# Kernel optimization log

Measured on AMD Instinct MI355X. Metric: run time of the kernel, lower is better.

Reference implementation:

```python
import jax, jax.numpy as jnp
import numpy as np

NQ = 4  # circuit is hard-wired to a 4-qubit ring
INV_SQRT2 = 1.0 / float(np.sqrt(2.0))


def _apply_1q(state, g, w):
    # state: [E,2,2,2,2]; g: [2,2] (shared) or [E,2,2] (per-edge)
    state = jnp.moveaxis(state, 1 + w, -1)
    sub = 'eab,e...b->e...a' if g.ndim == 3 else 'ab,e...b->e...a'
    state = jnp.einsum(sub, g, state)
    return jnp.moveaxis(state, -1, 1 + w)


def _apply_cry(state, theta, c, t):
    # controlled-RY(theta) with control wire c, target wire t; theta: [E]
    st = jnp.moveaxis(state, (1 + c, 1 + t), (-2, -1))  # [..., c, t]
    co = jnp.cos(theta / 2)[:, None, None]
    si = jnp.sin(theta / 2)[:, None, None]
    a = st[..., 1, 0]
    b = st[..., 1, 1]
    n0 = co * a - si * b
    n1 = si * a + co * b
    st = jnp.stack([jnp.stack([st[..., 0, 0], st[..., 0, 1]], axis=-1),
                    jnp.stack([n0, n1], axis=-1)], axis=-2)
    return jnp.moveaxis(st, (-2, -1), (1 + c, 1 + t))


def _simulate(q, k, params):
    # q, k: [E, NQ] rotation angles; params: [NQ, 3]
    E = q.shape[0]
    state = jnp.zeros((E, 2 ** NQ), jnp.complex64).at[:, 0].set(1.0)
    state = state.reshape((E,) + (2,) * NQ)
    # RY(query[i]) on wire i
    for w in range(NQ):
        c = jnp.cos(q[:, w] / 2)
        s = jnp.sin(q[:, w] / 2)
        g = jnp.stack([jnp.stack([c, -s], -1), jnp.stack([s, c], -1)], -2)
        state = _apply_1q(state, g.astype(jnp.complex64), w)
    # Hadamard on all wires
    H = jnp.array([[1, 1], [1, -1]], jnp.complex64) * INV_SQRT2
    for w in range(NQ):
        state = _apply_1q(state, H, w)
    # CRY(key[i]) on (i, (i+1)%NQ)
    for w in range(NQ):
        state = _apply_cry(state, k[:, w], w, (w + 1) % NQ)
    # Rot(phi, theta, omega) = RZ(omega) RY(theta) RZ(phi) on each wire
    for w in range(NQ):
        phi, th, om = params[w, 0], params[w, 1], params[w, 2]
        ct = jnp.cos(th / 2)
        st_ = jnp.sin(th / 2)
        g = jnp.stack([
            jnp.stack([jnp.exp(-1j * (phi + om) / 2) * ct, -jnp.exp(1j * (phi - om) / 2) * st_]),
            jnp.stack([jnp.exp(-1j * (phi - om) / 2) * st_, jnp.exp(1j * (phi + om) / 2) * ct]),
        ]).astype(jnp.complex64)
        state = _apply_1q(state, g, w)
    # <Z_i> expectation values
    p = jnp.abs(state) ** 2  # [E,2,2,2,2] float32
    exps = []
    for i in range(NQ):
        axes = tuple(a for a in range(1, 1 + NQ) if a != 1 + i)
        m = p.sum(axes)  # [E, 2]
        exps.append(m[:, 0] - m[:, 1])
    return jnp.stack(exps, -1).mean(-1)  # [E]


def setup_inputs() -> dict:
    key = jax.random.key(0)
    ks = jax.random.split(key, 7)
    N, D, E = 50000, 256, 800000
    node_features = jax.random.normal(ks[0], (N, D), jnp.float32)
    edge_index = jax.random.randint(ks[1], (2, E), 0, N)
    Wq = jax.random.normal(ks[2], (NQ, D), jnp.float32) / np.float32(np.sqrt(D))
    bq = jnp.zeros((NQ,), jnp.float32)
    Wk = jax.random.normal(ks[3], (NQ, D), jnp.float32) / np.float32(np.sqrt(D))
    bk = jnp.zeros((NQ,), jnp.float32)
    quantum_params = jax.random.normal(ks[4], (NQ, 3), jnp.float32) * 0.1
    return {'node_features': node_features, 'edge_index': edge_index,
            'Wq': Wq, 'bq': bq, 'Wk': Wk, 'bk': bk,
            'quantum_params': quantum_params}


def reference(node_features, edge_index, Wq, bq, Wk, bk, quantum_params):
    half_pi = np.float32(np.pi / 2)
    queries = jnp.tanh(node_features @ Wq.T + bq) * half_pi  # [N, NQ]
    keys = jnp.tanh(node_features @ Wk.T + bk) * half_pi     # [N, NQ]
    qe = queries[edge_index[0]]  # [E, NQ]
    ke = keys[edge_index[1]]     # [E, NQ]
    attn = _simulate(qe, ke, quantum_params)  # [E]
    return jax.nn.softmax(attn, axis=0)
```

## Files before the change

kernel.cpp:

```cpp
#include <hip/hip_runtime.h>
#include <math.h>

#define HALF_PI   1.57079632679489662f
#define INV_SQRT2 0.70710678118654752f
#define NPART     1024

__global__ __launch_bounds__(256) void node_qk(
        const float* __restrict__ feat,
        const float* __restrict__ Wq, const float* __restrict__ bq,
        const float* __restrict__ Wk, const float* __restrict__ bk,
        float* __restrict__ qtab, float* __restrict__ ktab, int N) {
    const int lane  = threadIdx.x & 63;
    const int wid   = (int)((blockIdx.x * blockDim.x + threadIdx.x) >> 6);
    const int nwid  = (int)((gridDim.x * blockDim.x) >> 6);

    float4 wq4[4], wk4[4];
    #pragma unroll
    for (int q = 0; q < 4; ++q) {
        wq4[q] = reinterpret_cast<const float4*>(Wq + q * 256)[lane];
        wk4[q] = reinterpret_cast<const float4*>(Wk + q * 256)[lane];
    }
    const int  g    = lane >> 3;
    const float bias = (g < 4) ? bq[g] : bk[g & 3];

    const bool hi  = (lane & 32) != 0;
    const bool s16 = (lane & 16) != 0;
    const bool s8  = (lane & 8)  != 0;

    for (int n = wid; n < N; n += nwid) {
        float4 f = reinterpret_cast<const float4*>(feat)[(size_t)n * 64 + lane];
        float acc[8];
        #pragma unroll
        for (int q = 0; q < 4; ++q) {
            acc[q]     = f.x * wq4[q].x + f.y * wq4[q].y + f.z * wq4[q].z + f.w * wq4[q].w;
            acc[4 + q] = f.x * wk4[q].x + f.y * wk4[q].y + f.z * wk4[q].z + f.w * wk4[q].w;
        }

        #pragma unroll
        for (int j = 0; j < 4; ++j) {
            float give = hi ? acc[j] : acc[j + 4];
            float r = __shfl_xor(give, 32, 64);
            acc[j]     += hi ? 0.f : r;
            acc[j + 4] += hi ? r : 0.f;
        }
        #pragma unroll
        for (int j = 0; j < 2; ++j) {
            float giveLow  = hi ? acc[6 + j] : acc[2 + j];
            float giveHigh = hi ? acc[4 + j] : acc[j];
            float give = s16 ? giveHigh : giveLow;
            float r = __shfl_xor(give, 16, 64);
            acc[j]     += (!hi && !s16) ? r : 0.f;
            acc[2 + j] += (!hi &&  s16) ? r : 0.f;
            acc[4 + j] += ( hi && !s16) ? r : 0.f;
            acc[6 + j] += ( hi &&  s16) ? r : 0.f;
        }
        float a_even = hi ? (s16 ? acc[6] : acc[4]) : (s16 ? acc[2] : acc[0]);
        float a_odd  = hi ? (s16 ? acc[7] : acc[5]) : (s16 ? acc[3] : acc[1]);
        float give3 = s8 ? a_even : a_odd;
        float r3 = __shfl_xor(give3, 8, 64);
        float v = (s8 ? a_odd : a_even) + r3;
        v += __shfl_xor(v, 4, 64);
        v += __shfl_xor(v, 2, 64);
        v += __shfl_xor(v, 1, 64);

        if ((lane & 7) == 0) {
            float t = tanhf(v + bias) * HALF_PI;
            if (g < 4) qtab[(size_t)n * 4 + g] = t;
            else       ktab[(size_t)n * 4 + (g & 3)] = t;
        }
    }
}

__global__ __launch_bounds__(256) void edge_attn(
        const int* __restrict__ ei,
        const float4* __restrict__ qtab, const float4* __restrict__ ktab,
        const float* __restrict__ qp,
        float* __restrict__ out, float* __restrict__ partial, int E) {
    __shared__ float scz[4], scx[4];
    __shared__ float red[256];
    const int tid = threadIdx.x;
    if (tid < 4) {
        float phi = qp[3 * tid + 0];
        float th  = qp[3 * tid + 1];
        float sth, cth;
        sincosf(th, &sth, &cth);
        scz[tid] = cth;
        scx[tid] = sth * cosf(phi);
    }
    __syncthreads();

    const int total = NPART * 256;
    float lsum = 0.f;
    #pragma unroll
    for (int i = 0; i < 4; ++i) {
        const int e = blockIdx.x * 256 + tid + i * total;
        if (e < E) {
            const int src = ei[e];
            const int dst = ei[E + e];
            float4 qv = qtab[src];
            float4 kv = ktab[dst];
            float qa[4] = {qv.x, qv.y, qv.z, qv.w};
            float ka[4] = {kv.x, kv.y, kv.z, kv.w};

            float u[4][2];
            #pragma unroll
            for (int w = 0; w < 4; ++w) {
                float s, c;
                __sincosf(qa[w] * 0.5f, &s, &c);
                u[w][0] = (c + s) * INV_SQRT2;
                u[w][1] = (c - s) * INV_SQRT2;
            }

            float a[16];
            #pragma unroll
            for (int x = 0; x < 16; ++x)
                a[x] = u[0][(x >> 3) & 1] * u[1][(x >> 2) & 1] *
                       u[2][(x >> 1) & 1] * u[3][x & 1];

            #pragma unroll
            for (int w = 0; w < 4; ++w) {
                float si, co;
                __sincosf(ka[w] * 0.5f, &si, &co);
                const int cb = 1 << (3 - w);
                const int tb = 1 << (3 - ((w + 1) & 3));
                #pragma unroll
                for (int x = 0; x < 16; ++x) {
                    if ((x & cb) && !(x & tb)) {
                        float a0 = a[x], a1 = a[x | tb];
                        a[x]      = co * a0 - si * a1;
                        a[x | tb] = si * a0 + co * a1;
                    }
                }
            }

            float attn = 0.f;
            #pragma unroll
            for (int q = 0; q < 4; ++q) {
                const int bit = 1 << (3 - q);
                float sz = 0.f, sx = 0.f;
                #pragma unroll
                for (int x = 0; x < 16; ++x) {
                    float pp = a[x] * a[x];
                    sz += (x & bit) ? -pp : pp;
                    if (!(x & bit)) sx += a[x] * a[x | bit];
                }
                attn += scz[q] * sz - scx[q] * (2.f * sx);
            }
            float ex = __expf(attn * 0.25f);
            out[e] = ex;
            lsum += ex;
        }
    }

    red[tid] = lsum;
    __syncthreads();
    #pragma unroll
    for (int s = 128; s > 0; s >>= 1) {
        if (tid < s) red[tid] += red[tid + s];
        __syncthreads();
    }
    if (tid == 0) partial[blockIdx.x] = red[0];
}

__global__ __launch_bounds__(256) void normalize_out(
        float* __restrict__ out, const float* __restrict__ partial, int E) {
    __shared__ float red[256];
    const int tid = threadIdx.x;
    float s = 0.f;
    #pragma unroll
    for (int k = 0; k < NPART / 256; ++k) s += partial[tid + k * 256];
    red[tid] = s;
    __syncthreads();
    #pragma unroll
    for (int st = 128; st > 0; st >>= 1) {
        if (tid < st) red[tid] += red[tid + st];
        __syncthreads();
    }
    const float inv = 1.f / red[0];

    const int total = (int)(gridDim.x * 256);
    for (int e = blockIdx.x * 256 + tid; e < E; e += total)
        out[e] *= inv;
}

extern "C" void kernel_launch(void* const* d_in, const int* in_sizes, int n_in,
                              void* d_out, int out_size, void* d_ws, size_t ws_size,
                              hipStream_t stream) {
    const float* feat = (const float*)d_in[0];
    const int*   ei   = (const int*)d_in[1];
    const float* Wq   = (const float*)d_in[2];
    const float* bq   = (const float*)d_in[3];
    const float* Wk   = (const float*)d_in[4];
    const float* bk   = (const float*)d_in[5];
    const float* qp   = (const float*)d_in[6];

    int D = in_sizes[2] / 4;
    int N = in_sizes[0] / D;
    int E = in_sizes[1] / 2;
    (void)D;

    float* ws      = (float*)d_ws;
    float* partial = ws;
    float* qtab    = ws + NPART;
    float* ktab    = qtab + (size_t)N * 4;
    float* out     = (float*)d_out;

    node_qk<<<2048, 256, 0, stream>>>(feat, Wq, bq, Wk, bk, qtab, ktab, N);
    edge_attn<<<NPART, 256, 0, stream>>>(ei, (const float4*)qtab, (const float4*)ktab,
                                         qp, out, partial, E);
    normalize_out<<<1024, 256, 0, stream>>>(out, partial, E);
}
```

Measured before the change: 34.27 us.

## Fuse three kernels into one persistent kernel with software grid barriers

Merges the node projection, edge attention and normalization kernels into a single persistent kernel of 512 blocks, separated by atomic-counter grid barriers. Exponentials stay in registers between the sum pass and the normalization pass, so the output is no longer written, re-read and rewritten. Edge indices are loaded as int4 and outputs are stored as float4. The design removes launch gaps and one output round trip, but it depends on all 512 blocks being co-resident and adds a memset plus spin-wait barrier costs.

```diff
diff --git a/kernel.cpp b/kernel.cpp
--- a/kernel.cpp
+++ b/kernel.cpp
@@ -3,82 +3,86 @@
 
 #define HALF_PI   1.57079632679489662f
 #define INV_SQRT2 0.70710678118654752f
-#define NPART     1024
-
-__global__ __launch_bounds__(256) void node_qk(
-        const float* __restrict__ feat,
+#define GB    512
+#define BT    256
+#define NTH   (GB * BT)
+#define MAXIT 2
+
+__device__ __forceinline__ void gridbar(int* cnt, int* flag) {
+    __syncthreads();
+    if (threadIdx.x == 0) {
+        int v = __hip_atomic_fetch_add(cnt, 1, __ATOMIC_ACQ_REL, __HIP_MEMORY_SCOPE_AGENT);
+        if (v == GB - 1) {
+            __hip_atomic_store(flag, 1, __ATOMIC_RELEASE, __HIP_MEMORY_SCOPE_AGENT);
+        } else {
+            while (__hip_atomic_load(flag, __ATOMIC_ACQUIRE, __HIP_MEMORY_SCOPE_AGENT) == 0) {
+                __builtin_amdgcn_s_sleep(2);
+            }
+        }
+    }
+    __syncthreads();
+}
+
+__device__ __forceinline__ float edge_ex(float4 qv, float4 kv,
+                                         const float* scz, const float* scx) {
+    float qa[4] = {qv.x, qv.y, qv.z, qv.w};
+    float ka[4] = {kv.x, kv.y, kv.z, kv.w};
+    float u[4][2];
+    #pragma unroll
+    for (int w = 0; w < 4; ++w) {
+        float s, c;
+        __sincosf(qa[w] * 0.5f, &s, &c);
+        u[w][0] = (c + s) * INV_SQRT2;
+        u[w][1] = (c - s) * INV_SQRT2;
+    }
+    float a[16];
+    #pragma unroll
+    for (int x = 0; x < 16; ++x)
+        a[x] = u[0][(x >> 3) & 1] * u[1][(x >> 2) & 1] *
+               u[2][(x >> 1) & 1] * u[3][x & 1];
+    #pragma unroll
+    for (int w = 0; w < 4; ++w) {
+        float si, co;
+        __sincosf(ka[w] * 0.5f, &si, &co);
+        const int cb = 1 << (3 - w);
+        const int tb = 1 << (3 - ((w + 1) & 3));
+        #pragma unroll
+        for (int x = 0; x < 16; ++x) {
+            if ((x & cb) && !(x & tb)) {
+                float a0 = a[x], a1 = a[x | tb];
+                a[x]      = co * a0 - si * a1;
+                a[x | tb] = si * a0 + co * a1;
+            }
+        }
+    }
+    float attn = 0.f;
+    #pragma unroll
+    for (int q = 0; q < 4; ++q) {
+        const int bit = 1 << (3 - q);
+        float sz = 0.f, sx = 0.f;
+        #pragma unroll
+        for (int x = 0; x < 16; ++x) {
+            float pp = a[x] * a[x];
+            sz += (x & bit) ? -pp : pp;
+            if (!(x & bit)) sx += a[x] * a[x | bit];
+        }
+        attn += scz[q] * sz - scx[q] * (2.f * sx);
+    }
+    return __expf(attn * 0.25f);
+}
+
+__global__ __launch_bounds__(BT, 2) void fused_qattn(
+        const float* __restrict__ feat, const int* __restrict__ ei,
         const float* __restrict__ Wq, const float* __restrict__ bq,
         const float* __restrict__ Wk, const float* __restrict__ bk,
-        float* __restrict__ qtab, float* __restrict__ ktab, int N) {
-    const int lane  = threadIdx.x & 63;
-    const int wid   = (int)((blockIdx.x * blockDim.x + threadIdx.x) >> 6);
-    const int nwid  = (int)((gridDim.x * blockDim.x) >> 6);
-
-    float4 wq4[4], wk4[4];
-    #pragma unroll
-    for (int q = 0; q < 4; ++q) {
-        wq4[q] = reinterpret_cast<const float4*>(Wq + q * 256)[lane];
-        wk4[q] = reinterpret_cast<const float4*>(Wk + q * 256)[lane];
-    }
-    const int  g    = lane >> 3;
-    const float bias = (g < 4) ? bq[g] : bk[g & 3];
-
-    const bool hi  = (lane & 32) != 0;
-    const bool s16 = (lane & 16) != 0;
-    const bool s8  = (lane & 8)  != 0;
-
-    for (int n = wid; n < N; n += nwid) {
-        float4 f = reinterpret_cast<const float4*>(feat)[(size_t)n * 64 + lane];
-        float acc[8];
-        #pragma unroll
-        for (int q = 0; q < 4; ++q) {
-            acc[q]     = f.x * wq4[q].x + f.y * wq4[q].y + f.z * wq4[q].z + f.w * wq4[q].w;
-            acc[4 + q] = f.x * wk4[q].x + f.y * wk4[q].y + f.z * wk4[q].z + f.w * wk4[q].w;
-        }
-
-        #pragma unroll
-        for (int j = 0; j < 4; ++j) {
-            float give = hi ? acc[j] : acc[j + 4];
-            float r = __shfl_xor(give, 32, 64);
-            acc[j]     += hi ? 0.f : r;
-            acc[j + 4] += hi ? r : 0.f;
-        }
-        #pragma unroll
-        for (int j = 0; j < 2; ++j) {
-            float giveLow  = hi ? acc[6 + j] : acc[2 + j];
-            float giveHigh = hi ? acc[4 + j] : acc[j];
-            float give = s16 ? giveHigh : giveLow;
-            float r = __shfl_xor(give, 16, 64);
-            acc[j]     += (!hi && !s16) ? r : 0.f;
-            acc[2 + j] += (!hi &&  s16) ? r : 0.f;
-            acc[4 + j] += ( hi && !s16) ? r : 0.f;
-            acc[6 + j] += ( hi &&  s16) ? r : 0.f;
-        }
-        float a_even = hi ? (s16 ? acc[6] : acc[4]) : (s16 ? acc[2] : acc[0]);
-        float a_odd  = hi ? (s16 ? acc[7] : acc[5]) : (s16 ? acc[3] : acc[1]);
-        float give3 = s8 ? a_even : a_odd;
-        float r3 = __shfl_xor(give3, 8, 64);
-        float v = (s8 ? a_odd : a_even) + r3;
-        v += __shfl_xor(v, 4, 64);
-        v += __shfl_xor(v, 2, 64);
-        v += __shfl_xor(v, 1, 64);
-
-        if ((lane & 7) == 0) {
-            float t = tanhf(v + bias) * HALF_PI;
-            if (g < 4) qtab[(size_t)n * 4 + g] = t;
-            else       ktab[(size_t)n * 4 + (g & 3)] = t;
-        }
-    }
-}
-
-__global__ __launch_bounds__(256) void edge_attn(
-        const int* __restrict__ ei,
-        const float4* __restrict__ qtab, const float4* __restrict__ ktab,
         const float* __restrict__ qp,
-        float* __restrict__ out, float* __restrict__ partial, int E) {
+        int* bar, float* partial, float* qtab, float* ktab,
+        float* __restrict__ out, int N, int E)
+{
     __shared__ float scz[4], scx[4];
-    __shared__ float red[256];
+    __shared__ float red[BT];
     const int tid = threadIdx.x;
+
     if (tid < 4) {
         float phi = qp[3 * tid + 0];
         float th  = qp[3 * tid + 1];
@@ -87,68 +91,115 @@
         scz[tid] = cth;
         scx[tid] = sth * cosf(phi);
     }
-    __syncthreads();
-
-    const int total = NPART * 256;
+
+    {
+        const int lane = tid & 63;
+        const int wid  = (blockIdx.x * BT + tid) >> 6;
+        const int nwid = NTH >> 6;
+
+        float4 wq4[4], wk4[4];
+        #pragma unroll
+        for (int q = 0; q < 4; ++q) {
+            wq4[q] = reinterpret_cast<const float4*>(Wq + q * 256)[lane];
+            wk4[q] = reinterpret_cast<const float4*>(Wk + q * 256)[lane];
+        }
+        const int   g    = lane >> 3;
+        const float bias = (g < 4) ? bq[g] : bk[g & 3];
+        const bool hi  = (lane & 32) != 0;
+        const bool s16 = (lane & 16) != 0;
+        const bool s8  = (lane & 8)  != 0;
+
+        for (int nb = wid * 2; nb < N; nb += nwid * 2) {
+            float4 f[2];
+            float  acc[2][8];
+            #pragma unroll
+            for (int p = 0; p < 2; ++p) {
+                const int n = nb + p;
+                if (n < N) f[p] = reinterpret_cast<const float4*>(feat)[(size_t)n * 64 + lane];
+                else       f[p] = make_float4(0.f, 0.f, 0.f, 0.f);
+                #pragma unroll
+                for (int q = 0; q < 4; ++q) {
+                    acc[p][q]     = f[p].x * wq4[q].x + f[p].y * wq4[q].y + f[p].z * wq4[q].z + f[p].w * wq4[q].w;
+                    acc[p][4 + q] = f[p].x * wk4[q].x + f[p].y * wk4[q].y + f[p].z * wk4[q].z + f[p].w * wk4[q].w;
+                }
+            }
+            #pragma unroll
+            for (int p = 0; p < 2; ++p) {
+                const int n = nb + p;
+                #pragma unroll
+                for (int j = 0; j < 4; ++j) {
+                    float give = hi ? acc[p][j] : acc[p][j + 4];
+                    float r = __shfl_xor(give, 32, 64);
+                    acc[p][j]     += hi ? 0.f : r;
+                    acc[p][j + 4] += hi ? r : 0.f;
+                }
+                #pragma unroll
+                for (int j = 0; j < 2; ++j) {
+                    float giveLow  = hi ? acc[p][6 + j] : acc[p][2 + j];
+                    float giveHigh = hi ? acc[p][4 + j] : acc[p][j];
+                    float give = s16 ? giveHigh : giveLow;
+                    float r = __shfl_xor(give, 16, 64);
+                    acc[p][j]     += (!hi && !s16) ? r : 0.f;
+                    acc[p][2 + j] += (!hi &&  s16) ? r : 0.f;
+                    acc[p][4 + j] += ( hi && !s16) ? r : 0.f;
+                    acc[p][6 + j] += ( hi &&  s16) ? r : 0.f;
+                }
+                float a_even = hi ? (s16 ? acc[p][6] : acc[p][4]) : (s16 ? acc[p][2] : acc[p][0]);
+                float a_odd  = hi ? (s16 ? acc[p][7] : acc[p][5]) : (s16 ? acc[p][3] : acc[p][1]);
+                float give3 = s8 ? a_even : a_odd;
+                float r3 = __shfl_xor(give3, 8, 64);
+                float v = (s8 ? a_odd : a_even) + r3;
+                v += __shfl_xor(v, 4, 64);
+                v += __shfl_xor(v, 2, 64);
+                v += __shfl_xor(v, 1, 64);
+
+                if (n < N && (lane & 7) == 0) {
+                    float t = tanhf(v + bias) * HALF_PI;
+                    if (g < 4) qtab[(size_t)n * 4 + g] = t;
+                    else       ktab[(size_t)n * 4 + (g & 3)] = t;
+                }
+            }
+        }
+    }
+
+    gridbar(bar + 0, bar + 32);
+
+    const float4* qtab4 = reinterpret_cast<const float4*>(qtab);
+    const float4* ktab4 = reinterpret_cast<const float4*>(ktab);
+    const int t4 = (blockIdx.x * BT + tid) * 4;
+    const bool dal = ((E & 3) == 0);
+
+    float ex[MAXIT][4];
     float lsum = 0.f;
     #pragma unroll
-    for (int i = 0; i < 4; ++i) {
-        const int e = blockIdx.x * 256 + tid + i * total;
-        if (e < E) {
-            const int src = ei[e];
-            const int dst = ei[E + e];
-            float4 qv = qtab[src];
-            float4 kv = ktab[dst];
-            float qa[4] = {qv.x, qv.y, qv.z, qv.w};
-            float ka[4] = {kv.x, kv.y, kv.z, kv.w};
-
-            float u[4][2];
-            #pragma unroll
-            for (int w = 0; w < 4; ++w) {
-                float s, c;
-                __sincosf(qa[w] * 0.5f, &s, &c);
-                u[w][0] = (c + s) * INV_SQRT2;
-                u[w][1] = (c - s) * INV_SQRT2;
-            }
-
-            float a[16];
-            #pragma unroll
-            for (int x = 0; x < 16; ++x)
-                a[x] = u[0][(x >> 3) & 1] * u[1][(x >> 2) & 1] *
-                       u[2][(x >> 1) & 1] * u[3][x & 1];
-
-            #pragma unroll
-            for (int w = 0; w < 4; ++w) {
-                float si, co;
-                __sincosf(ka[w] * 0.5f, &si, &co);
-                const int cb = 1 << (3 - w);
-                const int tb = 1 << (3 - ((w + 1) & 3));
-                #pragma unroll
-                for (int x = 0; x < 16; ++x) {
-                    if ((x & cb) && !(x & tb)) {
-                        float a0 = a[x], a1 = a[x | tb];
-                        a[x]      = co * a0 - si * a1;
-                        a[x | tb] = si * a0 + co * a1;
-                    }
-                }
-            }
-
-            float attn = 0.f;
-            #pragma unroll
-            for (int q = 0; q < 4; ++q) {
-                const int bit = 1 << (3 - q);
-                float sz = 0.f, sx = 0.f;
-                #pragma unroll
-                for (int x = 0; x < 16; ++x) {
-                    float pp = a[x] * a[x];
-                    sz += (x & bit) ? -pp : pp;
-                    if (!(x & bit)) sx += a[x] * a[x | bit];
-                }
-                attn += scz[q] * sz - scx[q] * (2.f * sx);
-            }
-            float ex = __expf(attn * 0.25f);
-            out[e] = ex;
-            lsum += ex;
+    for (int it = 0; it < MAXIT; ++it) {
+        const int base = t4 + it * (NTH * 4);
+        #pragma unroll
+        for (int j = 0; j < 4; ++j) ex[it][j] = 0.f;
+        if (base < E) {
+            int s[4], d[4];
+            if (dal && base + 3 < E) {
+                int4 sv = *reinterpret_cast<const int4*>(ei + base);
+                int4 dv = *reinterpret_cast<const int4*>(ei + E + base);
+                s[0] = sv.x; s[1] = sv.y; s[2] = sv.z; s[3] = sv.w;
+                d[0] = dv.x; d[1] = dv.y; d[2] = dv.z; d[3] = dv.w;
+            } else {
+                #pragma unroll
+                for (int j = 0; j < 4; ++j) {
+                    const int e = base + j;
+                    s[j] = (e < E) ? ei[e] : 0;
+                    d[j] = (e < E) ? ei[E + e] : 0;
+                }
+            }
+            #pragma unroll
+            for (int j = 0; j < 4; ++j) {
+                const int e = base + j;
+                if (e < E) {
+                    float v = edge_ex(qtab4[s[j]], ktab4[d[j]], scz, scx);
+                    ex[it][j] = v;
+                    lsum += v;
+                }
+            }
         }
     }
 
@@ -160,27 +211,34 @@
         __syncthreads();
     }
     if (tid == 0) partial[blockIdx.x] = red[0];
-}
-
-__global__ __launch_bounds__(256) void normalize_out(
-        float* __restrict__ out, const float* __restrict__ partial, int E) {
-    __shared__ float red[256];
-    const int tid = threadIdx.x;
-    float s = 0.f;
-    #pragma unroll
-    for (int k = 0; k < NPART / 256; ++k) s += partial[tid + k * 256];
-    red[tid] = s;
-    __syncthreads();
-    #pragma unroll
-    for (int st = 128; st > 0; st >>= 1) {
-        if (tid < st) red[tid] += red[tid + st];
+
+    gridbar(bar + 64, bar + 96);
+
+    float ps = partial[tid] + partial[tid + BT];
+    red[tid] = ps;
+    __syncthreads();
+    #pragma unroll
+    for (int s = 128; s > 0; s >>= 1) {
+        if (tid < s) red[tid] += red[tid + s];
         __syncthreads();
     }
     const float inv = 1.f / red[0];
 
-    const int total = (int)(gridDim.x * 256);
-    for (int e = blockIdx.x * 256 + tid; e < E; e += total)
-        out[e] *= inv;
+    #pragma unroll
+    for (int it = 0; it < MAXIT; ++it) {
+        const int base = t4 + it * (NTH * 4);
+        if (base + 3 < E) {
+            float4 o = make_float4(ex[it][0] * inv, ex[it][1] * inv,
+                                   ex[it][2] * inv, ex[it][3] * inv);
+            *reinterpret_cast<float4*>(out + base) = o;
+        } else {
+            #pragma unroll
+            for (int j = 0; j < 4; ++j) {
+                const int e = base + j;
+                if (e < E) out[e] = ex[it][j] * inv;
+            }
+        }
+    }
 }
 
 extern "C" void kernel_launch(void* const* d_in, const int* in_sizes, int n_in,
@@ -199,14 +257,13 @@
     int E = in_sizes[1] / 2;
     (void)D;
 
-    float* ws      = (float*)d_ws;
-    float* partial = ws;
-    float* qtab    = ws + NPART;
+    int*   bar     = (int*)d_ws;
+    float* partial = (float*)d_ws + 128;
+    float* qtab    = partial + GB;
     float* ktab    = qtab + (size_t)N * 4;
     float* out     = (float*)d_out;
 
-    node_qk<<<2048, 256, 0, stream>>>(feat, Wq, bq, Wk, bk, qtab, ktab, N);
-    edge_attn<<<NPART, 256, 0, stream>>>(ei, (const float4*)qtab, (const float4*)ktab,
-                                         qp, out, partial, E);
-    normalize_out<<<1024, 256, 0, stream>>>(out, partial, E);
-}
+    hipMemsetAsync(d_ws, 0, 512, stream);
+    fused_qattn<<<GB, BT, 0, stream>>>(feat, ei, Wq, bq, Wk, bk, qp,
+                                       bar, partial, qtab, ktab, out, N, E);
+}
```

New measurement: 108.2 us. +215.6%, slower.

## Fuse node projection, edge attention and softmax into one persistent kernel with grid barriers

Applied to the files above, without the earlier changes.

Merges the three kernels into a single persistent kernel of 2048 blocks that synchronises through hand-rolled atomic grid barriers. Edge exponentials stay in registers across the barrier, so the output is written once already normalised instead of written and then re-read and rescaled. This removes two kernel launch gaps and one full read-modify-write pass over the output. In exchange it adds a memset and two grid-wide spin barriers, and it relies on all blocks being co-resident, which is checked through an occupancy query with a fallback to the old three-kernel path.

```diff
diff --git a/kernel.cpp b/kernel.cpp
--- a/kernel.cpp
+++ b/kernel.cpp
@@ -3,7 +3,212 @@
 
 #define HALF_PI   1.57079632679489662f
 #define INV_SQRT2 0.70710678118654752f
-#define NPART     1024
+#define BT    256
+#define GBF   2048
+#define NTHF  (GBF * BT)
+#define NPART 1024
+
+__device__ __forceinline__ void gridbar(int* cnt) {
+    __syncthreads();
+    const int tid = threadIdx.x;
+    if (tid == 0) {
+        __hip_atomic_fetch_add(&cnt[(blockIdx.x & 63) * 16], 1,
+                               __ATOMIC_RELEASE, __HIP_MEMORY_SCOPE_AGENT);
+    }
+    if (tid < 64) {
+        int total;
+        for (;;) {
+            int v = __hip_atomic_load(&cnt[tid * 16],
+                                      __ATOMIC_ACQUIRE, __HIP_MEMORY_SCOPE_AGENT);
+            total = v;
+            #pragma unroll
+            for (int off = 32; off > 0; off >>= 1) total += __shfl_xor(total, off, 64);
+            if (total >= GBF) break;
+            __builtin_amdgcn_s_sleep(4);
+        }
+    }
+    __syncthreads();
+}
+
+__device__ __forceinline__ float edge_ex(float4 qv, float4 kv,
+                                         const float* scz, const float* scx) {
+    float qa[4] = {qv.x, qv.y, qv.z, qv.w};
+    float ka[4] = {kv.x, kv.y, kv.z, kv.w};
+    float u[4][2];
+    #pragma unroll
+    for (int w = 0; w < 4; ++w) {
+        float s, c;
+        __sincosf(qa[w] * 0.5f, &s, &c);
+        u[w][0] = (c + s) * INV_SQRT2;
+        u[w][1] = (c - s) * INV_SQRT2;
+    }
+    float a[16];
+    #pragma unroll
+    for (int x = 0; x < 16; ++x)
+        a[x] = u[0][(x >> 3) & 1] * u[1][(x >> 2) & 1] *
+               u[2][(x >> 1) & 1] * u[3][x & 1];
+    #pragma unroll
+    for (int w = 0; w < 4; ++w) {
+        float si, co;
+        __sincosf(ka[w] * 0.5f, &si, &co);
+        const int cb = 1 << (3 - w);
+        const int tb = 1 << (3 - ((w + 1) & 3));
+        #pragma unroll
+        for (int x = 0; x < 16; ++x) {
+            if ((x & cb) && !(x & tb)) {
+                float a0 = a[x], a1 = a[x | tb];
+                a[x]      = co * a0 - si * a1;
+                a[x | tb] = si * a0 + co * a1;
+            }
+        }
+    }
+    float attn = 0.f;
+    #pragma unroll
+    for (int q = 0; q < 4; ++q) {
+        const int bit = 1 << (3 - q);
+        float sz = 0.f, sx = 0.f;
+        #pragma unroll
+        for (int x = 0; x < 16; ++x) {
+            float pp = a[x] * a[x];
+            sz += (x & bit) ? -pp : pp;
+            if (!(x & bit)) sx += a[x] * a[x | bit];
+        }
+        attn += scz[q] * sz - scx[q] * (2.f * sx);
+    }
+    return __expf(attn * 0.25f);
+}
+
+__global__ __launch_bounds__(BT, 8) void fused_qattn(
+        const float* __restrict__ feat, const int* __restrict__ ei,
+        const float* __restrict__ Wq, const float* __restrict__ bq,
+        const float* __restrict__ Wk, const float* __restrict__ bk,
+        const float* __restrict__ qp,
+        int* barA, int* barB, float* partial, float* qtab, float* ktab,
+        float* __restrict__ out, int N, int E)
+{
+    __shared__ float scz[4], scx[4];
+    __shared__ float red[BT];
+    const int tid  = threadIdx.x;
+    const int gtid = blockIdx.x * BT + tid;
+
+    if (tid < 4) {
+        float phi = qp[3 * tid + 0];
+        float th  = qp[3 * tid + 1];
+        float sth, cth;
+        sincosf(th, &sth, &cth);
+        scz[tid] = cth;
+        scx[tid] = sth * cosf(phi);
+    }
+
+    {
+        const int lane = tid & 63;
+        const int wid  = gtid >> 6;
+        const int nwid = NTHF >> 6;
+
+        float4 wq4[4], wk4[4];
+        #pragma unroll
+        for (int q = 0; q < 4; ++q) {
+            wq4[q] = reinterpret_cast<const float4*>(Wq + q * 256)[lane];
+            wk4[q] = reinterpret_cast<const float4*>(Wk + q * 256)[lane];
+        }
+        const int   g    = lane >> 3;
+        const float bias = (g < 4) ? bq[g] : bk[g & 3];
+        const bool hi  = (lane & 32) != 0;
+        const bool s16 = (lane & 16) != 0;
+        const bool s8  = (lane & 8)  != 0;
+
+        for (int n = wid; n < N; n += nwid) {
+            float4 f = reinterpret_cast<const float4*>(feat)[(size_t)n * 64 + lane];
+            float acc[8];
+            #pragma unroll
+            for (int q = 0; q < 4; ++q) {
+                acc[q]     = f.x * wq4[q].x + f.y * wq4[q].y + f.z * wq4[q].z + f.w * wq4[q].w;
+                acc[4 + q] = f.x * wk4[q].x + f.y * wk4[q].y + f.z * wk4[q].z + f.w * wk4[q].w;
+            }
+            #pragma unroll
+            for (int j = 0; j < 4; ++j) {
+                float give = hi ? acc[j] : acc[j + 4];
+                float r = __shfl_xor(give, 32, 64);
+                acc[j]     += hi ? 0.f : r;
+                acc[j + 4] += hi ? r : 0.f;
+            }
+            #pragma unroll
+            for (int j = 0; j < 2; ++j) {
+                float giveLow  = hi ? acc[6 + j] : acc[2 + j];
+                float giveHigh = hi ? acc[4 + j] : acc[j];
+                float give = s16 ? giveHigh : giveLow;
+                float r = __shfl_xor(give, 16, 64);
+                acc[j]     += (!hi && !s16) ? r : 0.f;
+                acc[2 + j] += (!hi &&  s16) ? r : 0.f;
+                acc[4 + j] += ( hi && !s16) ? r : 0.f;
+                acc[6 + j] += ( hi &&  s16) ? r : 0.f;
+            }
+            float a_even = hi ? (s16 ? acc[6] : acc[4]) : (s16 ? acc[2] : acc[0]);
+            float a_odd  = hi ? (s16 ? acc[7] : acc[5]) : (s16 ? acc[3] : acc[1]);
+            float give3 = s8 ? a_even : a_odd;
+            float r3 = __shfl_xor(give3, 8, 64);
+            float v = (s8 ? a_odd : a_even) + r3;
+            v += __shfl_xor(v, 4, 64);
+            v += __shfl_xor(v, 2, 64);
+            v += __shfl_xor(v, 1, 64);
+
+            if ((lane & 7) == 0) {
+                float t = tanhf(v + bias) * HALF_PI;
+                if (g < 4) qtab[(size_t)n * 4 + g] = t;
+                else       ktab[(size_t)n * 4 + (g & 3)] = t;
+            }
+        }
+    }
+
+    gridbar(barA);
+
+    const float4* qtab4 = reinterpret_cast<const float4*>(qtab);
+    const float4* ktab4 = reinterpret_cast<const float4*>(ktab);
+
+    float ex[2];
+    float lsum = 0.f;
+    #pragma unroll
+    for (int it = 0; it < 2; ++it) {
+        const int e = gtid + it * NTHF;
+        ex[it] = 0.f;
+        if (e < E) {
+            const int s = ei[e];
+            const int d = ei[E + e];
+            float v = edge_ex(qtab4[s], ktab4[d], scz, scx);
+            ex[it] = v;
+            lsum += v;
+        }
+    }
+
+    red[tid] = lsum;
+    __syncthreads();
+    #pragma unroll
+    for (int s = 128; s > 0; s >>= 1) {
+        if (tid < s) red[tid] += red[tid + s];
+        __syncthreads();
+    }
+    if (tid == 0) partial[blockIdx.x] = red[0];
+
+    gridbar(barB);
+
+    float ps = 0.f;
+    #pragma unroll
+    for (int k = 0; k < GBF / BT; ++k) ps += partial[tid + k * BT];
+    red[tid] = ps;
+    __syncthreads();
+    #pragma unroll
+    for (int s = 128; s > 0; s >>= 1) {
+        if (tid < s) red[tid] += red[tid + s];
+        __syncthreads();
+    }
+    const float inv = 1.f / red[0];
+
+    #pragma unroll
+    for (int it = 0; it < 2; ++it) {
+        const int e = gtid + it * NTHF;
+        if (e < E) out[e] = ex[it] * inv;
+    }
+}
 
 __global__ __launch_bounds__(256) void node_qk(
         const float* __restrict__ feat,
@@ -13,7 +218,6 @@
     const int lane  = threadIdx.x & 63;
     const int wid   = (int)((blockIdx.x * blockDim.x + threadIdx.x) >> 6);
     const int nwid  = (int)((gridDim.x * blockDim.x) >> 6);
-
     float4 wq4[4], wk4[4];
     #pragma unroll
     for (int q = 0; q < 4; ++q) {
@@ -22,11 +226,9 @@
     }
     const int  g    = lane >> 3;
     const float bias = (g < 4) ? bq[g] : bk[g & 3];
-
     const bool hi  = (lane & 32) != 0;
     const bool s16 = (lane & 16) != 0;
     const bool s8  = (lane & 8)  != 0;
-
     for (int n = wid; n < N; n += nwid) {
         float4 f = reinterpret_cast<const float4*>(feat)[(size_t)n * 64 + lane];
         float acc[8];
@@ -35,7 +237,6 @@
             acc[q]     = f.x * wq4[q].x + f.y * wq4[q].y + f.z * wq4[q].z + f.w * wq4[q].w;
             acc[4 + q] = f.x * wk4[q].x + f.y * wk4[q].y + f.z * wk4[q].z + f.w * wk4[q].w;
         }
-
         #pragma unroll
         for (int j = 0; j < 4; ++j) {
             float give = hi ? acc[j] : acc[j + 4];
@@ -62,7 +263,6 @@
         v += __shfl_xor(v, 4, 64);
         v += __shfl_xor(v, 2, 64);
         v += __shfl_xor(v, 1, 64);
-
         if ((lane & 7) == 0) {
             float t = tanhf(v + bias) * HALF_PI;
             if (g < 4) qtab[(size_t)n * 4 + g] = t;
@@ -88,70 +288,17 @@
         scx[tid] = sth * cosf(phi);
     }
     __syncthreads();
-
     const int total = NPART * 256;
     float lsum = 0.f;
     #pragma unroll
     for (int i = 0; i < 4; ++i) {
         const int e = blockIdx.x * 256 + tid + i * total;
         if (e < E) {
-            const int src = ei[e];
-            const int dst = ei[E + e];
-            float4 qv = qtab[src];
-            float4 kv = ktab[dst];
-            float qa[4] = {qv.x, qv.y, qv.z, qv.w};
-            float ka[4] = {kv.x, kv.y, kv.z, kv.w};
-
-            float u[4][2];
-            #pragma unroll
-            for (int w = 0; w < 4; ++w) {
-                float s, c;
-                __sincosf(qa[w] * 0.5f, &s, &c);
-                u[w][0] = (c + s) * INV_SQRT2;
-                u[w][1] = (c - s) * INV_SQRT2;
-            }
-
-            float a[16];
-            #pragma unroll
-            for (int x = 0; x < 16; ++x)
-                a[x] = u[0][(x >> 3) & 1] * u[1][(x >> 2) & 1] *
-                       u[2][(x >> 1) & 1] * u[3][x & 1];
-
-            #pragma unroll
-            for (int w = 0; w < 4; ++w) {
-                float si, co;
-                __sincosf(ka[w] * 0.5f, &si, &co);
-                const int cb = 1 << (3 - w);
-                const int tb = 1 << (3 - ((w + 1) & 3));
-                #pragma unroll
-                for (int x = 0; x < 16; ++x) {
-                    if ((x & cb) && !(x & tb)) {
-                        float a0 = a[x], a1 = a[x | tb];
-                        a[x]      = co * a0 - si * a1;
-                        a[x | tb] = si * a0 + co * a1;
-                    }
-                }
-            }
-
-            float attn = 0.f;
-            #pragma unroll
-            for (int q = 0; q < 4; ++q) {
-                const int bit = 1 << (3 - q);
-                float sz = 0.f, sx = 0.f;
-                #pragma unroll
-                for (int x = 0; x < 16; ++x) {
-                    float pp = a[x] * a[x];
-                    sz += (x & bit) ? -pp : pp;
-                    if (!(x & bit)) sx += a[x] * a[x | bit];
-                }
-                attn += scz[q] * sz - scx[q] * (2.f * sx);
-            }
-            float ex = __expf(attn * 0.25f);
-            out[e] = ex;
-            lsum += ex;
-        }
-    }
-
+            float v = edge_ex(qtab[ei[e]], ktab[ei[E + e]], scz, scx);
+            out[e] = v;
+            lsum += v;
+        }
+    }
     red[tid] = lsum;
     __syncthreads();
     #pragma unroll
@@ -177,7 +324,6 @@
         __syncthreads();
     }
     const float inv = 1.f / red[0];
-
     const int total = (int)(gridDim.x * 256);
     for (int e = blockIdx.x * 256 + tid; e < E; e += total)
         out[e] *= inv;
@@ -199,14 +345,28 @@
     int E = in_sizes[1] / 2;
     (void)D;
 
-    float* ws      = (float*)d_ws;
-    float* partial = ws;
-    float* qtab    = ws + NPART;
+    int*   barA    = (int*)d_ws;
+    int*   barB    = barA + 1024;
+    float* partial = (float*)d_ws + 2048;
+    float* qtab    = (float*)d_ws + 4096;
     float* ktab    = qtab + (size_t)N * 4;
     float* out     = (float*)d_out;
 
-    node_qk<<<2048, 256, 0, stream>>>(feat, Wq, bq, Wk, bk, qtab, ktab, N);
-    edge_attn<<<NPART, 256, 0, stream>>>(ei, (const float4*)qtab, (const float4*)ktab,
-                                         qp, out, partial, E);
-    normalize_out<<<1024, 256, 0, stream>>>(out, partial, E);
-}
+    int maxB = 0;
+    hipError_t oerr = hipOccupancyMaxActiveBlocksPerMultiprocessor(
+        &maxB, reinterpret_cast<const void*>(&fused_qattn), BT, 0);
+    const bool fused_ok = (oerr == hipSuccess) && (maxB >= 8) &&
+                          (E <= 2 * NTHF);
+
+    if (fused_ok) {
+        hipMemsetAsync(d_ws, 0, 8192, stream);
+        fused_qattn<<<GBF, BT, 0, stream>>>(feat, ei, Wq, bq, Wk, bk, qp,
+                                            barA, barB, partial, qtab, ktab,
+                                            out, N, E);
+    } else {
+        node_qk<<<2048, 256, 0, stream>>>(feat, Wq, bq, Wk, bk, qtab, ktab, N);
+        edge_attn<<<NPART, 256, 0, stream>>>(ei, (const float4*)qtab,
+                                             (const float4*)ktab, qp, out, partial, E);
+        normalize_out<<<1024, 256, 0, stream>>>(out, partial, E);
+    }
+}
```

After: 34.30 us. About the same (+0.1%).
